# Performance work log

Measured on AMD Instinct MI355X. Metric: run time of the kernel, lower is better.

The kernel has to match this reference:

```python
import jax, jax.numpy as jnp
import numpy as np
import math

D_MODEL = 2048
N_HEADS = 16
HEAD_DIM = 128
ROPE_THETA = 10000.0


def apply_rope(x, pos, theta=ROPE_THETA):
    # x: [b, h, s, d], pos: [b, s] int
    d = x.shape[-1]
    inv_freq = 1.0 / (theta ** (jnp.arange(0, d, 2, dtype=jnp.float32) / d))  # [d/2]
    ang = pos.astype(jnp.float32)[:, None, :, None] * inv_freq  # [b,1,s,d/2]
    cos, sin = jnp.cos(ang), jnp.sin(ang)
    x1, x2 = x[..., 0::2], x[..., 1::2]
    out_even = x1 * cos - x2 * sin
    out_odd = x1 * sin + x2 * cos
    return jnp.stack([out_even, out_odd], axis=-1).reshape(x.shape)


def setup_inputs() -> dict:
    key = jax.random.key(0)
    ks = jax.random.split(key, 5)
    b, s = 2, 2048
    scale = 1.0 / math.sqrt(D_MODEL)
    x = jax.random.normal(ks[0], (b, s, D_MODEL), dtype=jnp.float32)
    Wq = jax.random.normal(ks[1], (D_MODEL, D_MODEL), dtype=jnp.float32) * scale
    Wk = jax.random.normal(ks[2], (D_MODEL, D_MODEL), dtype=jnp.float32) * scale
    Wv = jax.random.normal(ks[3], (D_MODEL, D_MODEL), dtype=jnp.float32) * scale
    Wo = jax.random.normal(ks[4], (D_MODEL, D_MODEL), dtype=jnp.float32) * scale
    token_positions = jnp.broadcast_to(jnp.arange(s, dtype=jnp.int32), (b, s))
    return {"x": x, "token_positions": token_positions, "Wq": Wq, "Wk": Wk, "Wv": Wv, "Wo": Wo}


def reference(x, token_positions, Wq, Wk, Wv, Wo):
    b, s, _ = x.shape
    h, d = N_HEADS, HEAD_DIM
    # QKV projections (Linear: x @ W.T), split heads: b s (h d) -> b h s d
    def proj(W):
        y = jnp.einsum('bse,fe->bsf', x, W)
        return y.reshape(b, s, h, d).transpose(0, 2, 1, 3)
    Q, K, V = proj(Wq), proj(Wk), proj(Wv)
    Q = apply_rope(Q, token_positions)
    K = apply_rope(K, token_positions)
    logits = jnp.einsum('bhqd,bhkd->bhqk', Q, K) / math.sqrt(d)
    causal = jnp.triu(jnp.ones((s, s), dtype=bool), 1)
    logits = jnp.where(causal, -jnp.inf, logits)
    attn = jax.nn.softmax(logits, axis=-1)
    ctx = jnp.einsum('bhqk,bhkd->bhqd', attn, V)
    ctx = ctx.transpose(0, 2, 1, 3).reshape(b, s, h * d)
    return jnp.einsum('bsf,ef->bse', ctx, Wo)
```

## Files before the change

### kernel.cpp

```cpp
#include <hip/hip_runtime.h>
#include <cstdint>
#include <cstddef>

typedef __bf16 bf16_t;
typedef __bf16 bf16x8 __attribute__((ext_vector_type(8)));
typedef float  f32x4  __attribute__((ext_vector_type(4)));

#define SEQ 2048
#define NH  16
#define HD  128
#define MM  4096
#define KK  2048

#define ASYNC16(g, l) __builtin_amdgcn_global_load_lds( \
    (const __attribute__((address_space(1))) void*)(g), \
    (__attribute__((address_space(3))) void*)(l), 16, 0, 0)

__global__ __launch_bounds__(256) void cast_all(const float* __restrict__ x,
                                                const float* __restrict__ Wq,
                                                const float* __restrict__ Wk,
                                                const float* __restrict__ Wv,
                                                const float* __restrict__ Wo,
                                                bf16_t* __restrict__ xb,
                                                bf16_t* __restrict__ wqkv,
                                                bf16_t* __restrict__ wob) {
    int i = blockIdx.x * 256 + threadIdx.x;
    const float* src;
    bf16_t* dst;
    int off;
    if (i < 2097152) { src = x; dst = xb; off = i; }
    else {
        int j = i - 2097152;
        int sel = j >> 20; off = j & 0xFFFFF;
        if (sel < 3) { src = (sel == 0) ? Wq : (sel == 1) ? Wk : Wv; dst = wqkv + (size_t)sel * 4194304; }
        else         { src = Wo; dst = wob; }
    }
    float4 v = ((const float4*)src)[off];
    union { bf16_t h[4]; uint2 u; } t;
    t.h[0] = (bf16_t)v.x; t.h[1] = (bf16_t)v.y;
    t.h[2] = (bf16_t)v.z; t.h[3] = (bf16_t)v.w;
    ((uint2*)dst)[off] = t.u;
}

union SMemU {
    struct { bf16_t A[3][4096]; bf16_t B[3][4096]; } st;
    bf16_t epi[64 * 136];
};

template<int MODE>
__device__ __forceinline__ void gemm_body(SMemU& sm,
                                          const bf16_t* __restrict__ A,
                                          const bf16_t* __restrict__ B,
                                          void* __restrict__ Cout,
                                          bf16_t* __restrict__ Kout,
                                          bf16_t* __restrict__ Vout,
                                          const int* __restrict__ pos) {
    const int tid = threadIdx.x;
    const int w = tid >> 6, l = tid & 63;
    const int lane16 = l & 15, quad = l >> 4;
    const int tm = blockIdx.y, tn = blockIdx.x;
    const int wm = w >> 1, wn = w & 1;

    const bf16_t* pA0 = A + (size_t)(tm * 128 + (2 * w + 0) * 16 + lane16) * KK + quad * 8;
    const bf16_t* pA1 = A + (size_t)(tm * 128 + (2 * w + 1) * 16 + lane16) * KK + quad * 8;
    const bf16_t* pB0 = B + (size_t)(tn * 128 + (2 * w + 0) * 16 + lane16) * KK + quad * 8;
    const bf16_t* pB1 = B + (size_t)(tn * 128 + (2 * w + 1) * 16 + lane16) * KK + quad * 8;

    f32x4 acc[4][4];
    for (int i = 0; i < 4; i++)
        for (int j = 0; j < 4; j++) acc[i][j] = (f32x4){0.f, 0.f, 0.f, 0.f};

    ASYNC16(pA0,      &sm.st.A[0][(2 * w + 0) * 512]);
    ASYNC16(pA1,      &sm.st.A[0][(2 * w + 1) * 512]);
    ASYNC16(pB0,      &sm.st.B[0][(2 * w + 0) * 512]);
    ASYNC16(pB1,      &sm.st.B[0][(2 * w + 1) * 512]);
    ASYNC16(pA0 + 32, &sm.st.A[1][(2 * w + 0) * 512]);
    ASYNC16(pA1 + 32, &sm.st.A[1][(2 * w + 1) * 512]);
    ASYNC16(pB0 + 32, &sm.st.B[1][(2 * w + 0) * 512]);
    ASYNC16(pB1 + 32, &sm.st.B[1][(2 * w + 1) * 512]);

    const bf16_t* qA0 = pA0 + 64;
    const bf16_t* qA1 = pA1 + 64;
    const bf16_t* qB0 = pB0 + 64;
    const bf16_t* qB1 = pB1 + 64;

    const int NT = KK / 32;
    int rdbuf = 0, stbuf = 2;
    for (int t = 0; t < NT; ++t) {
        if (t == NT - 1) { asm volatile("s_waitcnt vmcnt(0) lgkmcnt(0)" ::: "memory"); }
        else             { asm volatile("s_waitcnt vmcnt(4) lgkmcnt(0)" ::: "memory"); }
        __builtin_amdgcn_s_barrier();
        asm volatile("" ::: "memory");
        if (t + 2 < NT) {
            ASYNC16(qA0, &sm.st.A[stbuf][(2 * w + 0) * 512]);
            ASYNC16(qA1, &sm.st.A[stbuf][(2 * w + 1) * 512]);
            ASYNC16(qB0, &sm.st.B[stbuf][(2 * w + 0) * 512]);
            ASYNC16(qB1, &sm.st.B[stbuf][(2 * w + 1) * 512]);
            qA0 += 32; qA1 += 32; qB0 += 32; qB1 += 32;
            stbuf = (stbuf == 2) ? 0 : stbuf + 1;
        }
        const bf16_t* rA = &sm.st.A[rdbuf][wm * 2048 + l * 8];
        const bf16_t* rB = &sm.st.B[rdbuf][wn * 2048 + l * 8];
        bf16x8 af[4], bfr[4];
        for (int i = 0; i < 4; i++) af[i]  = *(const bf16x8*)(rA + i * 512);
        for (int j = 0; j < 4; j++) bfr[j] = *(const bf16x8*)(rB + j * 512);
        for (int i = 0; i < 4; i++)
            for (int j = 0; j < 4; j++)
                acc[i][j] = __builtin_amdgcn_mfma_f32_16x16x32_bf16(af[i], bfr[j], acc[i][j], 0, 0, 0);
        rdbuf = (rdbuf == 2) ? 0 : rdbuf + 1;
    }

    if (MODE == 1) {
        const int mbase = tm * 128 + wm * 64;
        const int nbase = tn * 128 + wn * 64;
        for (int i = 0; i < 4; i++)
            for (int j = 0; j < 4; j++) {
                const int n  = nbase + j * 16 + lane16;
                const int m0 = mbase + i * 16 + quad * 4;
                for (int r = 0; r < 4; r++)
                    ((float*)Cout)[(size_t)(m0 + r) * 2048 + n] = acc[i][j][r];
            }
        return;
    }

    const int mbase = tm * 128;
    const int nb    = tn * 128;
    const int sel   = nb >> 11;
    const int hh    = (nb & 2047) >> 7;
    const int bidx  = mbase >> 11;
    const int g  = tid >> 4;
    const int c8 = (tid & 15) * 8;

    if (sel < 2) {
        bf16_t* dstbase = ((sel == 0) ? (bf16_t*)Cout : Kout) +
                          (size_t)(bidx * NH + hh) * SEQ * HD;
        const float qs = (sel == 0) ? 0.08838834764831845f : 1.0f;
        for (int half = 0; half < 2; half++) {
            __syncthreads();
            if (wm == half) {
                for (int i = 0; i < 4; i++)
                    for (int j = 0; j < 4; j++)
                        for (int r = 0; r < 4; r++)
                            sm.epi[(i * 16 + quad * 4 + r) * 136 + wn * 64 + j * 16 + lane16] =
                                (bf16_t)acc[i][j][r];
            }
            __syncthreads();
            for (int p = 0; p < 4; p++) {
                const int rid = p * 16 + g;
                const int s = (mbase & 2047) + half * 64 + rid;
                bf16x8 v = *(const bf16x8*)&sm.epi[rid * 136 + c8];
                const float pp = (float)pos[bidx * SEQ + s];
                union { bf16_t h8[8]; uint4 u; } o;
                for (int t = 0; t < 4; t++) {
                    const int fi = (c8 >> 1) + t;
                    const float freq = exp2f(-(float)fi * 0.20762050593045857f);
                    const float ang = pp * freq;
                    const float sn = __sinf(ang), cs = __cosf(ang);
                    const float x1 = (float)v[2 * t], x2 = (float)v[2 * t + 1];
                    o.h8[2 * t]     = (bf16_t)((x1 * cs - x2 * sn) * qs);
                    o.h8[2 * t + 1] = (bf16_t)((x1 * sn + x2 * cs) * qs);
                }
                *(uint4*)(dstbase + (size_t)s * HD + c8) = o.u;
            }
        }
    } else {
        bf16_t* dstb = Vout + (size_t)(bidx * NH + hh) * HD * SEQ;
        const int s0 = mbase & 2047;
        for (int half = 0; half < 2; half++) {
            __syncthreads();
            if (wn == half) {
                for (int i = 0; i < 4; i++)
                    for (int j = 0; j < 4; j++) {
                        union { bf16_t h4[4]; uint2 u; } pk;
                        for (int r = 0; r < 4; r++) pk.h4[r] = (bf16_t)acc[i][j][r];
                        *(uint2*)&sm.epi[(j * 16 + lane16) * 136 + wm * 64 + i * 16 + quad * 4] = pk.u;
                    }
            }
            __syncthreads();
            for (int p = 0; p < 4; p++) {
                const int rid = p * 16 + g;
                const int d = half * 64 + rid;
                bf16x8 v = *(const bf16x8*)&sm.epi[rid * 136 + c8];
                *(uint4*)(dstb + (size_t)d * SEQ + s0 + c8) = *(const uint4*)&v;
            }
        }
    }
}

__global__ __launch_bounds__(256) void gemm_qkv(const bf16_t* __restrict__ A,
                                                const bf16_t* __restrict__ B,
                                                bf16_t* __restrict__ Qout,
                                                bf16_t* __restrict__ Kout,
                                                bf16_t* __restrict__ Vout,
                                                const int* __restrict__ pos) {
    __shared__ SMemU sm;
    gemm_body<3>(sm, A, B, (void*)Qout, Kout, Vout, pos);
}

__global__ __launch_bounds__(256) void gemm_out(const bf16_t* __restrict__ A,
                                                const bf16_t* __restrict__ B,
                                                float* __restrict__ Cout) {
    __shared__ SMemU sm;
    gemm_body<1>(sm, A, B, (void*)Cout, nullptr, nullptr, nullptr);
}

__global__ __launch_bounds__(256) void attn_kernel(const bf16_t* __restrict__ Q,
                                                   const bf16_t* __restrict__ K,
                                                   const bf16_t* __restrict__ Vt,
                                                   bf16_t* __restrict__ ctx) {
    const int flat = blockIdx.x;
    const int bh = flat & 31;
    const int bt = flat >> 5;
    const int h = bh & 15, b = bh >> 4;
    const bf16_t* Qh = Q  + (size_t)bh * SEQ * HD;
    const bf16_t* Kh = K  + (size_t)bh * SEQ * HD;
    const bf16_t* Vh = Vt + (size_t)bh * HD * SEQ;

    const int tid = threadIdx.x;
    const int w = tid >> 6, l = tid & 63;
    const int lane16 = l & 15, quad = l >> 4;

    __shared__ bf16_t kt[2][16 * 512];
    __shared__ bf16_t vt[2][16 * 512];
    __shared__ bf16_t pbuf[4][1024];

    for (int half = 0; half < 2; half++) {
        const int qt = half ? (31 - bt) : bt;
        const int q0 = qt * 64 + w * 16;

        bf16x8 qf[4];
        {
            const bf16_t* qrow = Qh + (size_t)(q0 + lane16) * HD + quad * 8;
            for (int kc = 0; kc < 4; kc++) qf[kc] = *(const bf16x8*)(qrow + kc * 32);
        }

        f32x4 o[8];
        for (int dt = 0; dt < 8; dt++) o[dt] = (f32x4){0.f, 0.f, 0.f, 0.f};
        float m_s = -INFINITY, l_s = 0.f;

        __syncthreads();
        for (int ii = 0; ii < 4; ii++) {
            const int f = w * 4 + ii;
            const int nt = f >> 2, kc = f & 3;
            ASYNC16(Kh + (size_t)(nt * 16 + lane16) * HD + kc * 32 + quad * 8, &kt[0][f * 512]);
            const int dt = f >> 1, kk = f & 1;
            ASYNC16(Vh + (size_t)(dt * 16 + lane16) * SEQ + kk * 32 + quad * 8, &vt[0][f * 512]);
        }

        int cur = 0;
        for (int kb = 0; kb <= qt; kb++) {
            const int k0 = kb * 64;
            __syncthreads();
            if (kb < qt) {
                const int kn = k0 + 64;
                for (int ii = 0; ii < 4; ii++) {
                    const int f = w * 4 + ii;
                    const int nt = f >> 2, kc = f & 3;
                    ASYNC16(Kh + (size_t)(kn + nt * 16 + lane16) * HD + kc * 32 + quad * 8,
                            &kt[1 - cur][f * 512]);
                    const int dt = f >> 1, kk = f & 1;
                    ASYNC16(Vh + (size_t)(dt * 16 + lane16) * SEQ + kn + kk * 32 + quad * 8,
                            &vt[1 - cur][f * 512]);
                }
            }
            const bf16_t* ktc = kt[cur];
            const bf16_t* vtc = vt[cur];

            f32x4 sacc[4];
            for (int nt = 0; nt < 4; nt++) sacc[nt] = (f32x4){0.f, 0.f, 0.f, 0.f};
            __builtin_amdgcn_s_setprio(1);
            for (int nt = 0; nt < 4; nt++)
                for (int kc = 0; kc < 4; kc++) {
                    bf16x8 kf = *(const bf16x8*)&ktc[(nt * 4 + kc) * 512 + l * 8];
                    sacc[nt] = __builtin_amdgcn_mfma_f32_16x16x32_bf16(kf, qf[kc], sacc[nt], 0, 0, 0);
                }
            __builtin_amdgcn_s_setprio(0);
            if (kb == qt) {
                const int qg = q0 + lane16;
                for (int nt = 0; nt < 4; nt++)
                    for (int r = 0; r < 4; r++) {
                        const int kg = k0 + nt * 16 + quad * 4 + r;
                        if (kg > qg) sacc[nt][r] = -INFINITY;
                    }
            }
            float rmnt[4];
            for (int nt = 0; nt < 4; nt++)
                rmnt[nt] = fmaxf(fmaxf(sacc[nt][0], sacc[nt][1]),
                                 fmaxf(sacc[nt][2], sacc[nt][3]));
            float rowmax = fmaxf(fmaxf(rmnt[0], rmnt[1]), fmaxf(rmnt[2], rmnt[3]));
            rowmax = fmaxf(rowmax, __shfl_xor(rowmax, 16, 64));
            rowmax = fmaxf(rowmax, __shfl_xor(rowmax, 32, 64));

            float a = 1.f;
            const bool noresc = __all(rowmax <= m_s + 8.f) != 0;
            if (!noresc) {
                const float mnew = fmaxf(m_s, rowmax);
                a = __expf(m_s - mnew);
                m_s = mnew;
            }
            float ssum = 0.f;
            for (int nt = 0; nt < 4; nt++) {
                union { bf16_t h4[4]; uint2 u; } pk;
                for (int r = 0; r < 4; r++) {
                    const float e = __expf(sacc[nt][r] - m_s);
                    ssum += e;
                    pk.h4[r] = (bf16_t)e;
                }
                const int addr = (nt >> 1) * 512 +
                                 (((nt & 1) * 2 + (quad >> 1)) * 16 + lane16) * 8 +
                                 (quad & 1) * 4;
                *(uint2*)&pbuf[w][addr] = pk.u;
            }
            ssum += __shfl_xor(ssum, 16, 64);
            ssum += __shfl_xor(ssum, 32, 64);
            l_s = l_s * a + ssum;

            if (!noresc) {
                float ar[4];
                for (int r = 0; r < 4; r++) ar[r] = __shfl(a, (quad << 2) | r, 16);
                for (int dt = 0; dt < 8; dt++)
                    for (int r = 0; r < 4; r++) o[dt][r] *= ar[r];
            }
            __builtin_amdgcn_s_setprio(1);
            for (int kk = 0; kk < 2; kk++) {
                bf16x8 pf = *(const bf16x8*)&pbuf[w][kk * 512 + l * 8];
                for (int dt = 0; dt < 8; dt++) {
                    bf16x8 vf = *(const bf16x8*)&vtc[(dt * 2 + kk) * 512 + l * 8];
                    o[dt] = __builtin_amdgcn_mfma_f32_16x16x32_bf16(pf, vf, o[dt], 0, 0, 0);
                }
            }
            __builtin_amdgcn_s_setprio(0);
            cur ^= 1;
        }

        float inv[4];
        for (int r = 0; r < 4; r++) inv[r] = 1.0f / __shfl(l_s, (quad << 2) | r, 16);
        for (int r = 0; r < 4; r++) {
            const int qg = q0 + quad * 4 + r;
            bf16_t* dst = ctx + ((size_t)(b * SEQ + qg)) * (NH * HD) + h * HD;
            for (int dt = 0; dt < 8; dt++)
                dst[dt * 16 + lane16] = (bf16_t)(o[dt][r] * inv[r]);
        }
        __syncthreads();
    }
}

extern "C" void kernel_launch(void* const* d_in, const int* in_sizes, int n_in,
                              void* d_out, int out_size, void* d_ws, size_t ws_size,
                              hipStream_t stream) {
    const float* x  = (const float*)d_in[0];
    const int* pos  = (const int*)d_in[1];
    const float* Wq = (const float*)d_in[2];
    const float* Wk = (const float*)d_in[3];
    const float* Wv = (const float*)d_in[4];
    const float* Wo = (const float*)d_in[5];

    char* ws = (char*)d_ws;
    bf16_t* xb   = (bf16_t*)(ws);
    bf16_t* wqkv = (bf16_t*)(ws + (16u << 20));
    bf16_t* wob  = (bf16_t*)(ws + (40u << 20));
    bf16_t* Qb   = (bf16_t*)(ws + (48u << 20));
    bf16_t* Kb   = (bf16_t*)(ws + (64u << 20));
    bf16_t* Vt   = (bf16_t*)(ws + (80u << 20));
    bf16_t* ctx  = (bf16_t*)(ws + (96u << 20));

    cast_all<<<24576, 256, 0, stream>>>(x, Wq, Wk, Wv, Wo, xb, wqkv, wob);

    dim3 gq(6144 / 128, MM / 128);
    gemm_qkv<<<gq, 256, 0, stream>>>(xb, wqkv, Qb, Kb, Vt, pos);

    attn_kernel<<<512, 256, 0, stream>>>(Qb, Kb, Vt, ctx);

    dim3 gg(2048 / 128, MM / 128);
    gemm_out<<<gg, 256, 0, stream>>>(ctx, wob, (float*)d_out);
}
```

Baseline: 455.1 us.

## Enlarge QKV GEMM tile to 256x256 with 512-thread blocks

The QKV projection GEMM moves from 128x128 tiles with 4 waves to 256x256 tiles with 8 waves, each wave computing a 128x64 sub-tile (8x4 MFMA accumulators). This halves global/LDS load traffic per FLOP and cuts the grid from 1536 to 384 blocks. The RoPE/transposed-V epilogue is rewritten to handle two heads per tile in four slices. Risks are higher register pressure (128 accumulator floats), more LDS per block lowering occupancy, and 384 blocks giving weaker load balance across CUs.

```diff
diff --git a/kernel.cpp b/kernel.cpp
--- a/kernel.cpp
+++ b/kernel.cpp
@@ -42,32 +42,31 @@
     ((uint2*)dst)[off] = t.u;
 }
 
-union SMemU {
-    struct { bf16_t A[3][4096]; bf16_t B[3][4096]; } st;
-    bf16_t epi[64 * 136];
+union SMem256 {
+    struct { bf16_t A[3][8192]; bf16_t B[3][8192]; } st;
+    bf16_t epi[64 * 264];
 };
 
-template<int MODE>
-__device__ __forceinline__ void gemm_body(SMemU& sm,
-                                          const bf16_t* __restrict__ A,
-                                          const bf16_t* __restrict__ B,
-                                          void* __restrict__ Cout,
-                                          bf16_t* __restrict__ Kout,
-                                          bf16_t* __restrict__ Vout,
-                                          const int* __restrict__ pos) {
+__global__ __launch_bounds__(512, 2) void gemm_qkv(const bf16_t* __restrict__ A,
+                                                   const bf16_t* __restrict__ B,
+                                                   bf16_t* __restrict__ Qout,
+                                                   bf16_t* __restrict__ Kout,
+                                                   bf16_t* __restrict__ Vout,
+                                                   const int* __restrict__ pos) {
+    __shared__ SMem256 sm;
     const int tid = threadIdx.x;
     const int w = tid >> 6, l = tid & 63;
     const int lane16 = l & 15, quad = l >> 4;
     const int tm = blockIdx.y, tn = blockIdx.x;
-    const int wm = w >> 1, wn = w & 1;
-
-    const bf16_t* pA0 = A + (size_t)(tm * 128 + (2 * w + 0) * 16 + lane16) * KK + quad * 8;
-    const bf16_t* pA1 = A + (size_t)(tm * 128 + (2 * w + 1) * 16 + lane16) * KK + quad * 8;
-    const bf16_t* pB0 = B + (size_t)(tn * 128 + (2 * w + 0) * 16 + lane16) * KK + quad * 8;
-    const bf16_t* pB1 = B + (size_t)(tn * 128 + (2 * w + 1) * 16 + lane16) * KK + quad * 8;
-
-    f32x4 acc[4][4];
-    for (int i = 0; i < 4; i++)
+    const int wm = w >> 2, wn = w & 3;
+
+    const bf16_t* pA0 = A + (size_t)(tm * 256 + (2 * w + 0) * 16 + lane16) * KK + quad * 8;
+    const bf16_t* pA1 = A + (size_t)(tm * 256 + (2 * w + 1) * 16 + lane16) * KK + quad * 8;
+    const bf16_t* pB0 = B + (size_t)(tn * 256 + (2 * w + 0) * 16 + lane16) * KK + quad * 8;
+    const bf16_t* pB1 = B + (size_t)(tn * 256 + (2 * w + 1) * 16 + lane16) * KK + quad * 8;
+
+    f32x4 acc[8][4];
+    for (int i = 0; i < 8; i++)
         for (int j = 0; j < 4; j++) acc[i][j] = (f32x4){0.f, 0.f, 0.f, 0.f};
 
     ASYNC16(pA0,      &sm.st.A[0][(2 * w + 0) * 512]);
@@ -99,6 +98,138 @@
             qA0 += 32; qA1 += 32; qB0 += 32; qB1 += 32;
             stbuf = (stbuf == 2) ? 0 : stbuf + 1;
         }
+        const bf16_t* rA = &sm.st.A[rdbuf][wm * 4096 + l * 8];
+        const bf16_t* rB = &sm.st.B[rdbuf][wn * 2048 + l * 8];
+        bf16x8 af[8], bfr[4];
+        for (int i = 0; i < 8; i++) af[i]  = *(const bf16x8*)(rA + i * 512);
+        for (int j = 0; j < 4; j++) bfr[j] = *(const bf16x8*)(rB + j * 512);
+        for (int i = 0; i < 8; i++)
+            for (int j = 0; j < 4; j++)
+                acc[i][j] = __builtin_amdgcn_mfma_f32_16x16x32_bf16(af[i], bfr[j], acc[i][j], 0, 0, 0);
+        rdbuf = (rdbuf == 2) ? 0 : rdbuf + 1;
+    }
+
+    const int mbase = tm * 256;
+    const int nb    = tn * 256;
+    const int sel   = nb >> 11;
+    const int hh0   = (nb & 2047) >> 7;
+    const int bidx  = mbase >> 11;
+    const int g   = tid >> 5;
+    const int c8  = (tid & 31) * 8;
+
+    if (sel < 2) {
+        bf16_t* base = ((sel == 0) ? Qout : Kout) + (size_t)(bidx * NH) * SEQ * HD;
+        const float qs = (sel == 0) ? 0.08838834764831845f : 1.0f;
+        for (int slice = 0; slice < 4; slice++) {
+            __syncthreads();
+            if (wm == (slice >> 1)) {
+                for (int i2 = 0; i2 < 4; i2++) {
+                    const int i = (slice & 1) * 4 + i2;
+                    for (int j = 0; j < 4; j++)
+                        for (int r = 0; r < 4; r++)
+                            sm.epi[(i2 * 16 + quad * 4 + r) * 264 + wn * 64 + j * 16 + lane16] =
+                                (bf16_t)acc[i][j][r];
+                }
+            }
+            __syncthreads();
+            const int head = hh0 + (c8 >> 7);
+            const int d0   = c8 & 127;
+            for (int p = 0; p < 4; p++) {
+                const int rid = p * 16 + g;
+                const int s = (mbase & 2047) + slice * 64 + rid;
+                bf16x8 v = *(const bf16x8*)&sm.epi[rid * 264 + c8];
+                const float pp = (float)pos[bidx * SEQ + s];
+                union { bf16_t h8[8]; uint4 u; } o;
+                for (int t = 0; t < 4; t++) {
+                    const int fi = (d0 >> 1) + t;
+                    const float freq = exp2f(-(float)fi * 0.20762050593045857f);
+                    const float ang = pp * freq;
+                    const float sn = __sinf(ang), cs = __cosf(ang);
+                    const float x1 = (float)v[2 * t], x2 = (float)v[2 * t + 1];
+                    o.h8[2 * t]     = (bf16_t)((x1 * cs - x2 * sn) * qs);
+                    o.h8[2 * t + 1] = (bf16_t)((x1 * sn + x2 * cs) * qs);
+                }
+                *(uint4*)(base + (size_t)(head * SEQ + s) * HD + d0) = o.u;
+            }
+        }
+    } else {
+        const int s0 = mbase & 2047;
+        for (int half = 0; half < 4; half++) {
+            __syncthreads();
+            if (wn == half) {
+                for (int i = 0; i < 8; i++)
+                    for (int j = 0; j < 4; j++) {
+                        union { bf16_t h4[4]; uint2 u; } pk;
+                        for (int r = 0; r < 4; r++) pk.h4[r] = (bf16_t)acc[i][j][r];
+                        *(uint2*)&sm.epi[(j * 16 + lane16) * 264 + wm * 128 + i * 16 + quad * 4] = pk.u;
+                    }
+            }
+            __syncthreads();
+            const int head = hh0 + (half >> 1);
+            bf16_t* dstb = Vout + (size_t)(bidx * NH + head) * HD * SEQ;
+            for (int p = 0; p < 4; p++) {
+                const int rid = p * 16 + g;
+                const int dh  = (half & 1) * 64 + rid;
+                bf16x8 v = *(const bf16x8*)&sm.epi[rid * 264 + c8];
+                *(uint4*)(dstb + (size_t)dh * SEQ + s0 + c8) = *(const uint4*)&v;
+            }
+        }
+    }
+}
+
+union SMemU {
+    struct { bf16_t A[3][4096]; bf16_t B[3][4096]; } st;
+    bf16_t epi[64 * 136];
+};
+
+__global__ __launch_bounds__(256) void gemm_out(const bf16_t* __restrict__ A,
+                                                const bf16_t* __restrict__ B,
+                                                float* __restrict__ Cout) {
+    __shared__ SMemU sm;
+    const int tid = threadIdx.x;
+    const int w = tid >> 6, l = tid & 63;
+    const int lane16 = l & 15, quad = l >> 4;
+    const int tm = blockIdx.y, tn = blockIdx.x;
+    const int wm = w >> 1, wn = w & 1;
+
+    const bf16_t* pA0 = A + (size_t)(tm * 128 + (2 * w + 0) * 16 + lane16) * KK + quad * 8;
+    const bf16_t* pA1 = A + (size_t)(tm * 128 + (2 * w + 1) * 16 + lane16) * KK + quad * 8;
+    const bf16_t* pB0 = B + (size_t)(tn * 128 + (2 * w + 0) * 16 + lane16) * KK + quad * 8;
+    const bf16_t* pB1 = B + (size_t)(tn * 128 + (2 * w + 1) * 16 + lane16) * KK + quad * 8;
+
+    f32x4 acc[4][4];
+    for (int i = 0; i < 4; i++)
+        for (int j = 0; j < 4; j++) acc[i][j] = (f32x4){0.f, 0.f, 0.f, 0.f};
+
+    ASYNC16(pA0,      &sm.st.A[0][(2 * w + 0) * 512]);
+    ASYNC16(pA1,      &sm.st.A[0][(2 * w + 1) * 512]);
+    ASYNC16(pB0,      &sm.st.B[0][(2 * w + 0) * 512]);
+    ASYNC16(pB1,      &sm.st.B[0][(2 * w + 1) * 512]);
+    ASYNC16(pA0 + 32, &sm.st.A[1][(2 * w + 0) * 512]);
+    ASYNC16(pA1 + 32, &sm.st.A[1][(2 * w + 1) * 512]);
+    ASYNC16(pB0 + 32, &sm.st.B[1][(2 * w + 0) * 512]);
+    ASYNC16(pB1 + 32, &sm.st.B[1][(2 * w + 1) * 512]);
+
+    const bf16_t* qA0 = pA0 + 64;
+    const bf16_t* qA1 = pA1 + 64;
+    const bf16_t* qB0 = pB0 + 64;
+    const bf16_t* qB1 = pB1 + 64;
+
+    const int NT = KK / 32;
+    int rdbuf = 0, stbuf = 2;
+    for (int t = 0; t < NT; ++t) {
+        if (t == NT - 1) { asm volatile("s_waitcnt vmcnt(0) lgkmcnt(0)" ::: "memory"); }
+        else             { asm volatile("s_waitcnt vmcnt(4) lgkmcnt(0)" ::: "memory"); }
+        __builtin_amdgcn_s_barrier();
+        asm volatile("" ::: "memory");
+        if (t + 2 < NT) {
+            ASYNC16(qA0, &sm.st.A[stbuf][(2 * w + 0) * 512]);
+            ASYNC16(qA1, &sm.st.A[stbuf][(2 * w + 1) * 512]);
+            ASYNC16(qB0, &sm.st.B[stbuf][(2 * w + 0) * 512]);
+            ASYNC16(qB1, &sm.st.B[stbuf][(2 * w + 1) * 512]);
+            qA0 += 32; qA1 += 32; qB0 += 32; qB1 += 32;
+            stbuf = (stbuf == 2) ? 0 : stbuf + 1;
+        }
         const bf16_t* rA = &sm.st.A[rdbuf][wm * 2048 + l * 8];
         const bf16_t* rB = &sm.st.B[rdbuf][wn * 2048 + l * 8];
         bf16x8 af[4], bfr[4];
@@ -110,98 +241,15 @@
         rdbuf = (rdbuf == 2) ? 0 : rdbuf + 1;
     }
 
-    if (MODE == 1) {
-        const int mbase = tm * 128 + wm * 64;
-        const int nbase = tn * 128 + wn * 64;
-        for (int i = 0; i < 4; i++)
-            for (int j = 0; j < 4; j++) {
-                const int n  = nbase + j * 16 + lane16;
-                const int m0 = mbase + i * 16 + quad * 4;
-                for (int r = 0; r < 4; r++)
-                    ((float*)Cout)[(size_t)(m0 + r) * 2048 + n] = acc[i][j][r];
-            }
-        return;
-    }
-
-    const int mbase = tm * 128;
-    const int nb    = tn * 128;
-    const int sel   = nb >> 11;
-    const int hh    = (nb & 2047) >> 7;
-    const int bidx  = mbase >> 11;
-    const int g  = tid >> 4;
-    const int c8 = (tid & 15) * 8;
-
-    if (sel < 2) {
-        bf16_t* dstbase = ((sel == 0) ? (bf16_t*)Cout : Kout) +
-                          (size_t)(bidx * NH + hh) * SEQ * HD;
-        const float qs = (sel == 0) ? 0.08838834764831845f : 1.0f;
-        for (int half = 0; half < 2; half++) {
-            __syncthreads();
-            if (wm == half) {
-                for (int i = 0; i < 4; i++)
-                    for (int j = 0; j < 4; j++)
-                        for (int r = 0; r < 4; r++)
-                            sm.epi[(i * 16 + quad * 4 + r) * 136 + wn * 64 + j * 16 + lane16] =
-                                (bf16_t)acc[i][j][r];
-            }
-            __syncthreads();
-            for (int p = 0; p < 4; p++) {
-                const int rid = p * 16 + g;
-                const int s = (mbase & 2047) + half * 64 + rid;
-                bf16x8 v = *(const bf16x8*)&sm.epi[rid * 136 + c8];
-                const float pp = (float)pos[bidx * SEQ + s];
-                union { bf16_t h8[8]; uint4 u; } o;
-                for (int t = 0; t < 4; t++) {
-                    const int fi = (c8 >> 1) + t;
-                    const float freq = exp2f(-(float)fi * 0.20762050593045857f);
-                    const float ang = pp * freq;
-                    const float sn = __sinf(ang), cs = __cosf(ang);
-                    const float x1 = (float)v[2 * t], x2 = (float)v[2 * t + 1];
-                    o.h8[2 * t]     = (bf16_t)((x1 * cs - x2 * sn) * qs);
-                    o.h8[2 * t + 1] = (bf16_t)((x1 * sn + x2 * cs) * qs);
-                }
-                *(uint4*)(dstbase + (size_t)s * HD + c8) = o.u;
-            }
-        }
-    } else {
-        bf16_t* dstb = Vout + (size_t)(bidx * NH + hh) * HD * SEQ;
-        const int s0 = mbase & 2047;
-        for (int half = 0; half < 2; half++) {
-            __syncthreads();
-            if (wn == half) {
-                for (int i = 0; i < 4; i++)
-                    for (int j = 0; j < 4; j++) {
-                        union { bf16_t h4[4]; uint2 u; } pk;
-                        for (int r = 0; r < 4; r++) pk.h4[r] = (bf16_t)acc[i][j][r];
-                        *(uint2*)&sm.epi[(j * 16 + lane16) * 136 + wm * 64 + i * 16 + quad * 4] = pk.u;
-                    }
-            }
-            __syncthreads();
-            for (int p = 0; p < 4; p++) {
-                const int rid = p * 16 + g;
-                const int d = half * 64 + rid;
-                bf16x8 v = *(const bf16x8*)&sm.epi[rid * 136 + c8];
-                *(uint4*)(dstb + (size_t)d * SEQ + s0 + c8) = *(const uint4*)&v;
-            }
-        }
-    }
-}
-
-__global__ __launch_bounds__(256) void gemm_qkv(const bf16_t* __restrict__ A,
-                                                const bf16_t* __restrict__ B,
-                                                bf16_t* __restrict__ Qout,
-                                                bf16_t* __restrict__ Kout,
-                                                bf16_t* __restrict__ Vout,
-                                                const int* __restrict__ pos) {
-    __shared__ SMemU sm;
-    gemm_body<3>(sm, A, B, (void*)Qout, Kout, Vout, pos);
-}
-
-__global__ __launch_bounds__(256) void gemm_out(const bf16_t* __restrict__ A,
-                                                const bf16_t* __restrict__ B,
-                                                float* __restrict__ Cout) {
-    __shared__ SMemU sm;
-    gemm_body<1>(sm, A, B, (void*)Cout, nullptr, nullptr, nullptr);
+    const int mbase = tm * 128 + wm * 64;
+    const int nbase = tn * 128 + wn * 64;
+    for (int i = 0; i < 4; i++)
+        for (int j = 0; j < 4; j++) {
+            const int n  = nbase + j * 16 + lane16;
+            const int m0 = mbase + i * 16 + quad * 4;
+            for (int r = 0; r < 4; r++)
+                Cout[(size_t)(m0 + r) * 2048 + n] = acc[i][j][r];
+        }
 }
 
 __global__ __launch_bounds__(256) void attn_kernel(const bf16_t* __restrict__ Q,
@@ -366,8 +414,8 @@
 
     cast_all<<<24576, 256, 0, stream>>>(x, Wq, Wk, Wv, Wo, xb, wqkv, wob);
 
-    dim3 gq(6144 / 128, MM / 128);
-    gemm_qkv<<<gq, 256, 0, stream>>>(xb, wqkv, Qb, Kb, Vt, pos);
+    dim3 gq(6144 / 256, MM / 256);
+    gemm_qkv<<<gq, 512, 0, stream>>>(xb, wqkv, Qb, Kb, Vt, pos);
 
     attn_kernel<<<512, 256, 0, stream>>>(Qb, Kb, Vt, ctx);
 
```

Measured after the change: 416.3 us. 1.09x faster.

## Use 256x128 tiles with 8 waves for QKV GEMM and interleave loads with MFMA

Applied to the files above, without the earlier changes.

The QKV projection GEMM moves to its own kernel with 512 threads and 256x128 output tiles, so each B tile is reused across twice as many rows and fewer blocks are launched. The K-loop is restructured to issue the async global-to-LDS prefetch for the next stage in between groups of MFMAs, with s_setprio raising wave priority during the matrix ops and a single barrier per iteration. The epilogue is adapted to four row slices for Q/K RoPE and a wider LDS staging buffer for the transposed V store. In exchange it uses more LDS per block and has fewer blocks to cover the GPU, which can lower occupancy and wave-level parallelism.

```diff
diff --git a/kernel.cpp b/kernel.cpp
--- a/kernel.cpp
+++ b/kernel.cpp
@@ -42,19 +42,175 @@
     ((uint2*)dst)[off] = t.u;
 }
 
+union SMemQ {
+    bf16_t st[3][24 * 512];
+    bf16_t epi[64 * 264];
+};
+
+__global__ __launch_bounds__(512, 4) void gemm_qkv(const bf16_t* __restrict__ A,
+                                                   const bf16_t* __restrict__ B,
+                                                   bf16_t* __restrict__ Qout,
+                                                   bf16_t* __restrict__ Kout,
+                                                   bf16_t* __restrict__ Vout,
+                                                   const int* __restrict__ pos) {
+    __shared__ SMemQ sm;
+    const int tid = threadIdx.x;
+    const int w = tid >> 6, l = tid & 63;
+    const int lane16 = l & 15, quad = l >> 4;
+    const int tm = blockIdx.y, tn = blockIdx.x;
+    const int wm = w >> 1, wn = w & 1;
+
+    const int f0 = 3 * w, f1 = 3 * w + 1, f2 = 3 * w + 2;
+    const bf16_t* p0 = (f0 < 16)
+        ? A + (size_t)(tm * 256 + f0 * 16 + lane16) * KK + quad * 8
+        : B + (size_t)(tn * 128 + (f0 - 16) * 16 + lane16) * KK + quad * 8;
+    const bf16_t* p1 = (f1 < 16)
+        ? A + (size_t)(tm * 256 + f1 * 16 + lane16) * KK + quad * 8
+        : B + (size_t)(tn * 128 + (f1 - 16) * 16 + lane16) * KK + quad * 8;
+    const bf16_t* p2 = (f2 < 16)
+        ? A + (size_t)(tm * 256 + f2 * 16 + lane16) * KK + quad * 8
+        : B + (size_t)(tn * 128 + (f2 - 16) * 16 + lane16) * KK + quad * 8;
+
+    f32x4 acc[4][4];
+    for (int i = 0; i < 4; i++)
+        for (int j = 0; j < 4; j++) acc[i][j] = (f32x4){0.f, 0.f, 0.f, 0.f};
+
+    ASYNC16(p0,      &sm.st[0][f0 * 512]);
+    ASYNC16(p1,      &sm.st[0][f1 * 512]);
+    ASYNC16(p2,      &sm.st[0][f2 * 512]);
+    ASYNC16(p0 + 32, &sm.st[1][f0 * 512]);
+    ASYNC16(p1 + 32, &sm.st[1][f1 * 512]);
+    ASYNC16(p2 + 32, &sm.st[1][f2 * 512]);
+    p0 += 64; p1 += 64; p2 += 64;
+
+    const int NT = KK / 32;
+    int rdbuf = 0, stbuf = 2;
+    for (int t = 0; t < NT; ++t) {
+        if (t == NT - 1) { asm volatile("s_waitcnt vmcnt(0) lgkmcnt(0)" ::: "memory"); }
+        else             { asm volatile("s_waitcnt vmcnt(3) lgkmcnt(0)" ::: "memory"); }
+        __builtin_amdgcn_s_barrier();
+        asm volatile("" ::: "memory");
+
+        const bf16_t* rA = &sm.st[rdbuf][(wm * 4 + 0) * 512 + l * 8];
+        const bf16_t* rB = &sm.st[rdbuf][(16 + wn * 4) * 512 + l * 8];
+        const bool pf = (t + 2 < NT);
+        bf16_t* sb = &sm.st[stbuf][0];
+
+        bf16x8 af0 = *(const bf16x8*)(rA + 0 * 512);
+        bf16x8 af1 = *(const bf16x8*)(rA + 1 * 512);
+        bf16x8 bf0 = *(const bf16x8*)(rB + 0 * 512);
+        bf16x8 bf1 = *(const bf16x8*)(rB + 1 * 512);
+        if (pf) ASYNC16(p0, sb + f0 * 512);
+        __builtin_amdgcn_s_setprio(1);
+        acc[0][0] = __builtin_amdgcn_mfma_f32_16x16x32_bf16(af0, bf0, acc[0][0], 0, 0, 0);
+        acc[0][1] = __builtin_amdgcn_mfma_f32_16x16x32_bf16(af0, bf1, acc[0][1], 0, 0, 0);
+        acc[1][0] = __builtin_amdgcn_mfma_f32_16x16x32_bf16(af1, bf0, acc[1][0], 0, 0, 0);
+        acc[1][1] = __builtin_amdgcn_mfma_f32_16x16x32_bf16(af1, bf1, acc[1][1], 0, 0, 0);
+        __builtin_amdgcn_s_setprio(0);
+
+        bf16x8 af2 = *(const bf16x8*)(rA + 2 * 512);
+        bf16x8 af3 = *(const bf16x8*)(rA + 3 * 512);
+        if (pf) ASYNC16(p1, sb + f1 * 512);
+        __builtin_amdgcn_s_setprio(1);
+        acc[2][0] = __builtin_amdgcn_mfma_f32_16x16x32_bf16(af2, bf0, acc[2][0], 0, 0, 0);
+        acc[2][1] = __builtin_amdgcn_mfma_f32_16x16x32_bf16(af2, bf1, acc[2][1], 0, 0, 0);
+        acc[3][0] = __builtin_amdgcn_mfma_f32_16x16x32_bf16(af3, bf0, acc[3][0], 0, 0, 0);
+        acc[3][1] = __builtin_amdgcn_mfma_f32_16x16x32_bf16(af3, bf1, acc[3][1], 0, 0, 0);
+        __builtin_amdgcn_s_setprio(0);
+
+        bf16x8 bf2 = *(const bf16x8*)(rB + 2 * 512);
+        bf16x8 bf3 = *(const bf16x8*)(rB + 3 * 512);
+        if (pf) ASYNC16(p2, sb + f2 * 512);
+        __builtin_amdgcn_s_setprio(1);
+        acc[0][2] = __builtin_amdgcn_mfma_f32_16x16x32_bf16(af0, bf2, acc[0][2], 0, 0, 0);
+        acc[0][3] = __builtin_amdgcn_mfma_f32_16x16x32_bf16(af0, bf3, acc[0][3], 0, 0, 0);
+        acc[1][2] = __builtin_amdgcn_mfma_f32_16x16x32_bf16(af1, bf2, acc[1][2], 0, 0, 0);
+        acc[1][3] = __builtin_amdgcn_mfma_f32_16x16x32_bf16(af1, bf3, acc[1][3], 0, 0, 0);
+        acc[2][2] = __builtin_amdgcn_mfma_f32_16x16x32_bf16(af2, bf2, acc[2][2], 0, 0, 0);
+        acc[2][3] = __builtin_amdgcn_mfma_f32_16x16x32_bf16(af2, bf3, acc[2][3], 0, 0, 0);
+        acc[3][2] = __builtin_amdgcn_mfma_f32_16x16x32_bf16(af3, bf2, acc[3][2], 0, 0, 0);
+        acc[3][3] = __builtin_amdgcn_mfma_f32_16x16x32_bf16(af3, bf3, acc[3][3], 0, 0, 0);
+        __builtin_amdgcn_s_setprio(0);
+
+        if (pf) { p0 += 32; p1 += 32; p2 += 32; }
+        rdbuf = (rdbuf == 2) ? 0 : rdbuf + 1;
+        stbuf = (stbuf == 2) ? 0 : stbuf + 1;
+    }
+
+    const int mbase = tm * 256;
+    const int nb    = tn * 128;
+    const int sel   = nb >> 11;
+    const int hh    = (nb & 2047) >> 7;
+    const int bidx  = mbase >> 11;
+
+    if (sel < 2) {
+        bf16_t* dstbase = ((sel == 0) ? Qout : Kout) + (size_t)(bidx * NH + hh) * SEQ * HD;
+        const float qs = (sel == 0) ? 0.08838834764831845f : 1.0f;
+        const int g  = tid >> 4;
+        const int c8 = (tid & 15) * 8;
+        for (int slice = 0; slice < 4; slice++) {
+            __syncthreads();
+            if (wm == slice) {
+                for (int i = 0; i < 4; i++)
+                    for (int j = 0; j < 4; j++)
+                        for (int r = 0; r < 4; r++)
+                            sm.epi[(i * 16 + quad * 4 + r) * 136 + wn * 64 + j * 16 + lane16] =
+                                (bf16_t)acc[i][j][r];
+            }
+            __syncthreads();
+            for (int p = 0; p < 2; p++) {
+                const int rid = p * 32 + g;
+                const int s = (mbase & 2047) + slice * 64 + rid;
+                bf16x8 v = *(const bf16x8*)&sm.epi[rid * 136 + c8];
+                const float pp = (float)pos[bidx * SEQ + s];
+                union { bf16_t h8[8]; uint4 u; } o;
+                for (int t = 0; t < 4; t++) {
+                    const int fi = (c8 >> 1) + t;
+                    const float freq = exp2f(-(float)fi * 0.20762050593045857f);
+                    const float ang = pp * freq;
+                    const float sn = __sinf(ang), cs = __cosf(ang);
+                    const float x1 = (float)v[2 * t], x2 = (float)v[2 * t + 1];
+                    o.h8[2 * t]     = (bf16_t)((x1 * cs - x2 * sn) * qs);
+                    o.h8[2 * t + 1] = (bf16_t)((x1 * sn + x2 * cs) * qs);
+                }
+                *(uint4*)(dstbase + (size_t)s * HD + c8) = o.u;
+            }
+        }
+    } else {
+        bf16_t* dstb = Vout + (size_t)(bidx * NH + hh) * HD * SEQ;
+        const int s0 = mbase & 2047;
+        const int g5  = tid >> 5;
+        const int c8v = (tid & 31) * 8;
+        for (int h2 = 0; h2 < 2; h2++) {
+            __syncthreads();
+            if (wn == h2) {
+                for (int i = 0; i < 4; i++)
+                    for (int j = 0; j < 4; j++) {
+                        union { bf16_t h4[4]; uint2 u; } pk;
+                        for (int r = 0; r < 4; r++) pk.h4[r] = (bf16_t)acc[i][j][r];
+                        *(uint2*)&sm.epi[(j * 16 + lane16) * 264 + wm * 64 + i * 16 + quad * 4] = pk.u;
+                    }
+            }
+            __syncthreads();
+            for (int p = 0; p < 4; p++) {
+                const int rid = p * 16 + g5;
+                const int d   = h2 * 64 + rid;
+                bf16x8 v = *(const bf16x8*)&sm.epi[rid * 264 + c8v];
+                *(uint4*)(dstb + (size_t)d * SEQ + s0 + c8v) = *(const uint4*)&v;
+            }
+        }
+    }
+}
+
 union SMemU {
     struct { bf16_t A[3][4096]; bf16_t B[3][4096]; } st;
     bf16_t epi[64 * 136];
 };
 
-template<int MODE>
-__device__ __forceinline__ void gemm_body(SMemU& sm,
-                                          const bf16_t* __restrict__ A,
-                                          const bf16_t* __restrict__ B,
-                                          void* __restrict__ Cout,
-                                          bf16_t* __restrict__ Kout,
-                                          bf16_t* __restrict__ Vout,
-                                          const int* __restrict__ pos) {
+__global__ __launch_bounds__(256) void gemm_out(const bf16_t* __restrict__ A,
+                                                const bf16_t* __restrict__ B,
+                                                float* __restrict__ Cout) {
+    __shared__ SMemU sm;
     const int tid = threadIdx.x;
     const int w = tid >> 6, l = tid & 63;
     const int lane16 = l & 15, quad = l >> 4;
@@ -110,98 +266,15 @@
         rdbuf = (rdbuf == 2) ? 0 : rdbuf + 1;
     }
 
-    if (MODE == 1) {
-        const int mbase = tm * 128 + wm * 64;
-        const int nbase = tn * 128 + wn * 64;
-        for (int i = 0; i < 4; i++)
-            for (int j = 0; j < 4; j++) {
-                const int n  = nbase + j * 16 + lane16;
-                const int m0 = mbase + i * 16 + quad * 4;
-                for (int r = 0; r < 4; r++)
-                    ((float*)Cout)[(size_t)(m0 + r) * 2048 + n] = acc[i][j][r];
-            }
-        return;
-    }
-
-    const int mbase = tm * 128;
-    const int nb    = tn * 128;
-    const int sel   = nb >> 11;
-    const int hh    = (nb & 2047) >> 7;
-    const int bidx  = mbase >> 11;
-    const int g  = tid >> 4;
-    const int c8 = (tid & 15) * 8;
-
-    if (sel < 2) {
-        bf16_t* dstbase = ((sel == 0) ? (bf16_t*)Cout : Kout) +
-                          (size_t)(bidx * NH + hh) * SEQ * HD;
-        const float qs = (sel == 0) ? 0.08838834764831845f : 1.0f;
-        for (int half = 0; half < 2; half++) {
-            __syncthreads();
-            if (wm == half) {
-                for (int i = 0; i < 4; i++)
-                    for (int j = 0; j < 4; j++)
-                        for (int r = 0; r < 4; r++)
-                            sm.epi[(i * 16 + quad * 4 + r) * 136 + wn * 64 + j * 16 + lane16] =
-                                (bf16_t)acc[i][j][r];
-            }
-            __syncthreads();
-            for (int p = 0; p < 4; p++) {
-                const int rid = p * 16 + g;
-                const int s = (mbase & 2047) + half * 64 + rid;
-                bf16x8 v = *(const bf16x8*)&sm.epi[rid * 136 + c8];
-                const float pp = (float)pos[bidx * SEQ + s];
-                union { bf16_t h8[8]; uint4 u; } o;
-                for (int t = 0; t < 4; t++) {
-                    const int fi = (c8 >> 1) + t;
-                    const float freq = exp2f(-(float)fi * 0.20762050593045857f);
-                    const float ang = pp * freq;
-                    const float sn = __sinf(ang), cs = __cosf(ang);
-                    const float x1 = (float)v[2 * t], x2 = (float)v[2 * t + 1];
-                    o.h8[2 * t]     = (bf16_t)((x1 * cs - x2 * sn) * qs);
-                    o.h8[2 * t + 1] = (bf16_t)((x1 * sn + x2 * cs) * qs);
-                }
-                *(uint4*)(dstbase + (size_t)s * HD + c8) = o.u;
-            }
-        }
-    } else {
-        bf16_t* dstb = Vout + (size_t)(bidx * NH + hh) * HD * SEQ;
-        const int s0 = mbase & 2047;
-        for (int half = 0; half < 2; half++) {
-            __syncthreads();
-            if (wn == half) {
-                for (int i = 0; i < 4; i++)
-                    for (int j = 0; j < 4; j++) {
-                        union { bf16_t h4[4]; uint2 u; } pk;
-                        for (int r = 0; r < 4; r++) pk.h4[r] = (bf16_t)acc[i][j][r];
-                        *(uint2*)&sm.epi[(j * 16 + lane16) * 136 + wm * 64 + i * 16 + quad * 4] = pk.u;
-                    }
-            }
-            __syncthreads();
-            for (int p = 0; p < 4; p++) {
-                const int rid = p * 16 + g;
-                const int d = half * 64 + rid;
-                bf16x8 v = *(const bf16x8*)&sm.epi[rid * 136 + c8];
-                *(uint4*)(dstb + (size_t)d * SEQ + s0 + c8) = *(const uint4*)&v;
-            }
-        }
-    }
-}
-
-__global__ __launch_bounds__(256) void gemm_qkv(const bf16_t* __restrict__ A,
-                                                const bf16_t* __restrict__ B,
-                                                bf16_t* __restrict__ Qout,
-                                                bf16_t* __restrict__ Kout,
-                                                bf16_t* __restrict__ Vout,
-                                                const int* __restrict__ pos) {
-    __shared__ SMemU sm;
-    gemm_body<3>(sm, A, B, (void*)Qout, Kout, Vout, pos);
-}
-
-__global__ __launch_bounds__(256) void gemm_out(const bf16_t* __restrict__ A,
-                                                const bf16_t* __restrict__ B,
-                                                float* __restrict__ Cout) {
-    __shared__ SMemU sm;
-    gemm_body<1>(sm, A, B, (void*)Cout, nullptr, nullptr, nullptr);
+    const int mbase = tm * 128 + wm * 64;
+    const int nbase = tn * 128 + wn * 64;
+    for (int i = 0; i < 4; i++)
+        for (int j = 0; j < 4; j++) {
+            const int n  = nbase + j * 16 + lane16;
+            const int m0 = mbase + i * 16 + quad * 4;
+            for (int r = 0; r < 4; r++)
+                Cout[(size_t)(m0 + r) * 2048 + n] = acc[i][j][r];
+        }
 }
 
 __global__ __launch_bounds__(256) void attn_kernel(const bf16_t* __restrict__ Q,
@@ -366,8 +439,8 @@
 
     cast_all<<<24576, 256, 0, stream>>>(x, Wq, Wk, Wv, Wo, xb, wqkv, wob);
 
-    dim3 gq(6144 / 128, MM / 128);
-    gemm_qkv<<<gq, 256, 0, stream>>>(xb, wqkv, Qb, Kb, Vt, pos);
+    dim3 gq(6144 / 128, MM / 256);
+    gemm_qkv<<<gq, 512, 0, stream>>>(xb, wqkv, Qb, Kb, Vt, pos);
 
     attn_kernel<<<512, 256, 0, stream>>>(Qb, Kb, Vt, ctx);
 
```

Result: faster. 416.9 us (-8.4%).
